# Performance work log

Hardware: AMD Instinct MI355X
Metric: run time of the kernel (lower is better)

Reference implementation:

```python
import jax, jax.numpy as jnp
import numpy as np

B, L, H, P = 4, 8192, 256, 256


def discretize(log_real, imag, log_Delta, B_real, B_imag):
    # Lambda = -exp(log_real) + i*imag ; ZOH discretization
    Lr = -jnp.exp(log_real)
    Li = imag
    Delta = jnp.exp(log_Delta)
    ad = Lr * Delta
    bd = Li * Delta
    exp_ad = jnp.exp(ad)
    Lbar_r = exp_ad * jnp.cos(bd)
    Lbar_i = exp_ad * jnp.sin(bd)
    denom = jnp.maximum(Lr * Lr + Li * Li, 1e-12)
    inv_Lr = Lr / denom
    inv_Li = -Li / denom
    diff_r = Lbar_r - 1.0
    diff_i = Lbar_i
    coeff_r = inv_Lr * diff_r - inv_Li * diff_i
    coeff_i = inv_Lr * diff_i + inv_Li * diff_r
    B_bar_r = coeff_r[:, None] * B_real - coeff_i[:, None] * B_imag
    B_bar_i = coeff_r[:, None] * B_imag + coeff_i[:, None] * B_real
    return Lbar_r, Lbar_i, B_bar_r, B_bar_i


def binop(ei, ej):
    Ar_i, Ai_i, xr_i, xi_i = ei
    Ar_j, Ai_j, xr_j, xi_j = ej
    return (Ar_j * Ar_i - Ai_j * Ai_i,
            Ar_j * Ai_i + Ai_j * Ar_i,
            Ar_j * xr_i - Ai_j * xi_i + xr_j,
            Ar_j * xi_i + Ai_j * xr_i + xi_j)


def apply_ssm(Lbar_r, Lbar_i, B_bar_r, B_bar_i, C_real, C_imag, D, x):
    # x: (B,L,H), B_bar: (P,H), C: (H,P)
    Bu_r = jnp.einsum('blh,ph->blp', x, B_bar_r)
    Bu_i = jnp.einsum('blh,ph->blp', x, B_bar_i)
    A_r = jnp.broadcast_to(Lbar_r, Bu_r.shape)
    A_i = jnp.broadcast_to(Lbar_i, Bu_i.shape)
    _, _, xs_r, xs_i = jax.lax.associative_scan(binop, (A_r, A_i, Bu_r, Bu_i), axis=1)
    ys = jnp.einsum('blp,hp->blh', xs_r, C_real) - jnp.einsum('blp,hp->blh', xs_i, C_imag)
    return ys + D * x


def s5(log_real, imag, log_Delta, B_real, B_imag, C_real, C_imag, D, x):
    Lbar_r, Lbar_i, B_bar_r, B_bar_i = discretize(log_real, imag, log_Delta, B_real, B_imag)
    y = apply_ssm(Lbar_r, Lbar_i, B_bar_r, B_bar_i, C_real, C_imag, D, x)
    return jax.nn.gelu(y, approximate=False)


def setup_inputs() -> dict:
    key = jax.random.key(0)
    ks = jax.random.split(key, 17)
    std_b = 1.0 / H ** 0.5
    std_c = 1.0 / P ** 0.5
    def params(ki):
        k = jax.random.split(ks[ki], 8)
        return dict(
            log_real=jax.random.normal(k[0], (P,), jnp.float32) * 0.5,
            imag=jax.random.normal(k[1], (P,), jnp.float32),
            log_Delta=jnp.zeros((P,), jnp.float32),
            B_real=jax.random.normal(k[2], (P, H), jnp.float32) * std_b,
            B_imag=jax.random.normal(k[3], (P, H), jnp.float32) * std_b,
            C_real=jax.random.normal(k[4], (H, P), jnp.float32) * std_c,
            C_imag=jax.random.normal(k[5], (H, P), jnp.float32) * std_c,
            D=jnp.ones((H,), jnp.float32),
        )
    f = params(1)
    b = params(2)
    inp = {'x': jax.random.normal(ks[0], (B, L, H), jnp.float32)}
    for name, v in f.items():
        inp['fwd_' + name] = v
    for name, v in b.items():
        inp['bwd_' + name] = v
    return inp


def reference(x,
              fwd_log_real, fwd_imag, fwd_log_Delta, fwd_B_real, fwd_B_imag,
              fwd_C_real, fwd_C_imag, fwd_D,
              bwd_log_real, bwd_imag, bwd_log_Delta, bwd_B_real, bwd_B_imag,
              bwd_C_real, bwd_C_imag, bwd_D):
    x_flip = jnp.flip(x, axis=1)
    y_f = s5(fwd_log_real, fwd_imag, fwd_log_Delta, fwd_B_real, fwd_B_imag,
             fwd_C_real, fwd_C_imag, fwd_D, x)
    y_b = s5(bwd_log_real, bwd_imag, bwd_log_Delta, bwd_B_real, bwd_B_imag,
             bwd_C_real, bwd_C_imag, bwd_D, x_flip)
    return y_f + jnp.flip(y_b, axis=1)
```

## Files before the change

kernel.cpp:

```cpp
#include <hip/hip_runtime.h>
#include <math.h>

#define B_DIM 4
#define L_DIM 8192
#define H_DIM 256
#define P_DIM 256
#define M_DIM (B_DIM * L_DIM)
#define NC 64
#define LC 128

typedef __attribute__((ext_vector_type(8))) short bf16x8;
typedef __attribute__((ext_vector_type(4))) float f32x4;

static __device__ __forceinline__ float bf2f(unsigned int u) {
    union { unsigned int i; float f; } v; v.i = u << 16; return v.f;
}
static __device__ __forceinline__ unsigned short f2bf(float f) {
    union { float f; unsigned int i; } v; v.f = f;
    unsigned int r = v.i + 0x7FFFu + ((v.i >> 16) & 1u);
    return (unsigned short)(r >> 16);
}
static __device__ __forceinline__ float gelu_f(float x) {
    float z = 0.7978845608028654f * (x + 0.044715f * x * x * x);
    float e = __expf(2.0f * z);
    float t = 1.0f - 2.0f / (e + 1.0f);
    return 0.5f * x * (1.0f + t);
}
static __device__ __forceinline__ void async_load16(const void* g, void* l) {
    __builtin_amdgcn_global_load_lds(
        (const __attribute__((address_space(1))) unsigned int*)g,
        (__attribute__((address_space(3))) unsigned int*)l, 16, 0, 0);
}
static __device__ __forceinline__ float2 cmul2(float2 a, float2 b) {
    return make_float2(a.x * b.x - a.y * b.y, a.x * b.y + a.y * b.x);
}
static __device__ __forceinline__ float2 csq2(float2 a) {
    return make_float2(a.x * a.x - a.y * a.y, 2.f * a.x * a.y);
}
static __device__ __forceinline__ float2 cmad(float2 A, float2 s, float2 z) {
    return make_float2(A.x * s.x - A.y * s.y + z.x, A.x * s.y + A.y * s.x + z.y);
}

__global__ void prep_kernel(const float* fLr, const float* fIm, const float* fLd,
                            const float* fBr, const float* fBi,
                            const float* fCr, const float* fCi,
                            const float* bLr, const float* bIm, const float* bLd,
                            const float* bBr, const float* bBi,
                            const float* bCr, const float* bCi,
                            const float4* __restrict__ x4, ushort4* __restrict__ xb,
                            unsigned short* Bmat, unsigned short* B3, float2* LbarWS) {
    int gid = blockIdx.x * 256 + threadIdx.x;
    if (gid < 2097152) {
        float4 v = x4[gid];
        ushort4 o;
        o.x = f2bf(v.x); o.y = f2bf(v.y); o.z = f2bf(v.z); o.w = f2bf(v.w);
        xb[gid] = o;
        return;
    }
    int g1 = gid - 2097152;
    if (g1 < 262144) {
        int k = g1 >> 8, h = g1 & 255;
        int d = k >> 9, pc = k & 511, p = pc >> 1, comp = pc & 1;
        const float* LR = d ? bLr : fLr;
        const float* IM = d ? bIm : fIm;
        const float* LD = d ? bLd : fLd;
        const float* BR = d ? bBr : fBr;
        const float* BI = d ? bBi : fBi;
        float Lr = -expf(LR[p]);
        float Li = IM[p];
        float Delta = expf(LD[p]);
        float ea = expf(Lr * Delta);
        float bd = Li * Delta;
        float Lbr = ea * cosf(bd);
        float Lbi = ea * sinf(bd);
        float denom = fmaxf(Lr * Lr + Li * Li, 1e-12f);
        float ivr = Lr / denom, ivi = -Li / denom;
        float dr = Lbr - 1.0f, di = Lbi;
        float cr = ivr * dr - ivi * di;
        float ci = ivr * di + ivi * dr;
        float br = BR[p * 256 + h], bi = BI[p * 256 + h];
        float val = comp ? (cr * bi + ci * br) : (cr * br - ci * bi);
        Bmat[g1] = f2bf(val);
    } else if (g1 < 524288) {
        int g2 = g1 - 262144;
        int d = g2 >> 17;
        int rem = g2 & 131071;
        int h = rem >> 9;
        int kk = rem & 511;
        int p = kk >> 1, comp = kk & 1;
        const float* CR = d ? bCr : fCr;
        const float* CI = d ? bCi : fCi;
        float val = comp ? -CI[h * 256 + p] : CR[h * 256 + p];
        B3[g2] = f2bf(val);
    } else if (g1 < 524800) {
        int g2 = g1 - 524288;
        int d = g2 >> 8, p = g2 & 255;
        const float* LR = d ? bLr : fLr;
        const float* IM = d ? bIm : fIm;
        const float* LD = d ? bLd : fLd;
        float Lr = -expf(LR[p]); float Li = IM[p]; float Delta = expf(LD[p]);
        float ea = expf(Lr * Delta); float bd = Li * Delta;
        LbarWS[g2] = make_float2(ea * cosf(bd), ea * sinf(bd));
    }
}

__global__ __launch_bounds__(256, 2) void k1_gemm(const unsigned short* __restrict__ A,
                                                  const unsigned short* __restrict__ Bm,
                                                  unsigned short* __restrict__ Bu,
                                                  const float2* __restrict__ Lbar,
                                                  float2* __restrict__ carry,
                                                  float2* __restrict__ Usub) {
    __shared__ unsigned short SH[16384];
    __shared__ float2 Sbuf2[64][4];
    int tid = threadIdx.x;
    int lane = tid & 63, wv = tid >> 6;
    int wm = (wv >> 1) * 64, wn = (wv & 1) * 64;
    int Mb = blockIdx.x * 128, Nb = blockIdx.y * 128;
    int lr = lane >> 3;
    int swz = ((lane & 7) ^ lr) * 8;
    f32x4 acc[4][4];
#pragma unroll
    for (int i = 0; i < 4; i++)
#pragma unroll
        for (int j = 0; j < 4; j++) acc[i][j] = (f32x4){0.f, 0.f, 0.f, 0.f};
    int mrow = lane & 15, quad = lane >> 4;
    for (int kb = 0; kb < 256; kb += 64) {
#pragma unroll
        for (int ch = wv; ch < 16; ch += 4) {
            int r = ch * 8 + lr;
            async_load16(A  + (size_t)(Mb + r) * 256 + kb + swz, (char*)SH + ch * 1024);
            async_load16(Bm + (size_t)(Nb + r) * 256 + kb + swz, (char*)SH + 16384 + ch * 1024);
        }
        __syncthreads();
#pragma unroll
        for (int kk = 0; kk < 64; kk += 32) {
            bf16x8 af[4], bfr[4];
#pragma unroll
            for (int i = 0; i < 4; i++) {
                int rr = wm + 16 * i + mrow;
                af[i] = *(const bf16x8*)&SH[rr * 64 + ((((kk >> 3) + quad) ^ (rr & 7)) << 3)];
            }
#pragma unroll
            for (int j = 0; j < 4; j++) {
                int rr = wn + 16 * j + mrow;
                bfr[j] = *(const bf16x8*)&SH[8192 + rr * 64 + ((((kk >> 3) + quad) ^ (rr & 7)) << 3)];
            }
#pragma unroll
            for (int i = 0; i < 4; i++)
#pragma unroll
                for (int j = 0; j < 4; j++)
                    acc[i][j] = __builtin_amdgcn_mfma_f32_16x16x32_bf16(af[i], bfr[j], acc[i][j], 0, 0, 0);
        }
        __syncthreads();
    }
    unsigned short* Cs = SH;
#pragma unroll
    for (int i = 0; i < 4; i++)
#pragma unroll
        for (int j = 0; j < 4; j++)
#pragma unroll
            for (int r = 0; r < 4; r++) {
                int row = wm + 16 * i + quad * 4 + r;
                int col = wn + 16 * j + mrow;
                Cs[row * 128 + col] = f2bf(acc[i][j][r]);
            }
    __syncthreads();
#pragma unroll
    for (int it = 0; it < 8; it++) {
        int o = tid * 16 + it * 4096;
        int row = o >> 8, colb = o & 255;
        uint4 v = *(const uint4*)((const char*)Cs + o);
        *(uint4*)((char*)Bu + (size_t)(Mb + row) * 2048 + (size_t)Nb * 2 + colb) = v;
    }
    int d = Nb >> 9;
    int b = Mb >> 13;
    int c = (Mb >> 7) & 63;
    float2 s = make_float2(0.f, 0.f);
    float2 A2 = make_float2(0.f, 0.f);
    float2 snap[3];
    snap[0] = snap[1] = snap[2] = make_float2(0.f, 0.f);
    int p = 0;
    if (tid < 128) {
        int j = tid & 63, half = tid >> 6;
        p = ((Nb & 511) >> 1) + j;
        A2 = Lbar[d * 256 + p];
        const unsigned int* C32 = (const unsigned int*)Cs;
        int r0 = half * 64;
        if (d == 0) {
            for (int t = 0; t < 64; t++) {
                unsigned int v = C32[(r0 + t) * 64 + j];
                float2 z = make_float2(bf2f(v & 0xffffu), bf2f(v >> 16));
                s = cmad(A2, s, z);
                if ((t & 15) == 15 && t < 63) snap[t >> 4] = s;
            }
        } else {
            for (int t = 63; t >= 0; t--) {
                unsigned int v = C32[(r0 + t) * 64 + j];
                float2 z = make_float2(bf2f(v & 0xffffu), bf2f(v >> 16));
                s = cmad(A2, s, z);
                if ((t & 15) == 0 && t > 0) snap[(t >> 4) - 1] = s;
            }
        }
        if (half == 1) {
            Sbuf2[j][0] = snap[0]; Sbuf2[j][1] = snap[1];
            Sbuf2[j][2] = snap[2]; Sbuf2[j][3] = s;
        }
    }
    __syncthreads();
    if (tid < 64) {
        float2 h1a = Sbuf2[tid][0], h1b = Sbuf2[tid][1], h1c = Sbuf2[tid][2], S1 = Sbuf2[tid][3];
        float2 a16 = A2;
#pragma unroll
        for (int k = 0; k < 4; k++) a16 = csq2(a16);
        float2 a32 = csq2(a16);
        float2 a48 = cmul2(a32, a16);
        float2 a64 = csq2(a32);
        float2 S0 = s;
        float2 Uq[8];
        float2 cfull;
        float2 zero = make_float2(0.f, 0.f);
        if (d == 0) {
            Uq[0] = zero;  Uq[1] = snap[0]; Uq[2] = snap[1]; Uq[3] = snap[2];
            Uq[4] = S0;
            Uq[5] = cmad(a16, S0, h1a);
            Uq[6] = cmad(a32, S0, h1b);
            Uq[7] = cmad(a48, S0, h1c);
            cfull = cmad(a64, S0, S1);
        } else {
            Uq[7] = zero;
            Uq[6] = h1c;
            Uq[5] = h1b;
            Uq[4] = h1a;
            Uq[3] = S1;
            Uq[2] = cmad(a16, S1, snap[2]);
            Uq[1] = cmad(a32, S1, snap[1]);
            Uq[0] = cmad(a48, S1, snap[0]);
            cfull = cmad(a64, S1, S0);
        }
        size_t cidx = ((size_t)(d * 4 + b) * NC + c) * 256 + p;
        carry[cidx] = cfull;
        size_t ub = (((size_t)(d * 4 + b) * NC + c) * 8) * 256 + p;
#pragma unroll
        for (int q = 0; q < 8; q++) Usub[ub + (size_t)q * 256] = Uq[q];
    }
}

static __device__ __forceinline__ void k3_half(const unsigned short* __restrict__ XS,
                                               const unsigned short* __restrict__ B3h,
                                               unsigned short* As, unsigned short* Bs,
                                               float2* UL, const float2* Ptab, const float2* LbarL,
                                               const float2* __restrict__ Uchunk,
                                               int Mb, int Hb, int coff, int d,
                                               int wm, int wn, int mrow, int quad,
                                               int lr, int swz, int wv, int tid,
                                               f32x4 (&acc)[4][4]) {
#pragma unroll
    for (int it = 0; it < 4; it++)
        async_load16((const char*)Uchunk + (size_t)(wv * 4 + it) * 1024 + (size_t)(tid & 63) * 16,
                     (char*)UL + (wv * 4 + it) * 1024);
    int j = tid & 31, q = tid >> 5;
    int r0 = q * 16;
    for (int kb = 0; kb < 512; kb += 64) {
#pragma unroll
        for (int ch = wv; ch < 16; ch += 4) {
            int r = ch * 8 + lr;
            async_load16(XS + (size_t)(Mb + r) * 1024 + coff + kb + swz, (char*)As + ch * 1024);
            async_load16(B3h + (size_t)(Hb + r) * 512 + kb + swz, (char*)Bs + ch * 1024);
        }
        __syncthreads();
        {
            int p = (kb >> 1) + j;
            float2 Ac = LbarL[d * 256 + p];
            float2 P  = Ptab[d * 256 + p];
            float2 U  = UL[q * 256 + p];
            int e = d ? (7 - q) : q;
            float2 ap = make_float2(1.f, 0.f);
            float2 bp = Ac;
#pragma unroll
            for (int k = 0; k < 4; k++) bp = csq2(bp);
            if (e & 1) ap = cmul2(ap, bp);
            bp = csq2(bp);
            if (e & 2) ap = cmul2(ap, bp);
            bp = csq2(bp);
            if (e & 4) ap = cmul2(ap, bp);
            float2 s = cmad(ap, P, U);
            unsigned int* A32 = (unsigned int*)As;
            unsigned int zb[16];
#pragma unroll
            for (int t = 0; t < 16; t++) {
                int row = r0 + t;
                zb[t] = A32[row * 32 + (((j >> 2) ^ (row & 7)) << 2) + (j & 3)];
            }
            if (d == 0) {
#pragma unroll
                for (int t = 0; t < 16; t++) {
                    float2 z = make_float2(bf2f(zb[t] & 0xffffu), bf2f(zb[t] >> 16));
                    s = cmad(Ac, s, z);
                    zb[t] = (unsigned int)f2bf(s.x) | ((unsigned int)f2bf(s.y) << 16);
                }
            } else {
#pragma unroll
                for (int t = 15; t >= 0; t--) {
                    float2 z = make_float2(bf2f(zb[t] & 0xffffu), bf2f(zb[t] >> 16));
                    s = cmad(Ac, s, z);
                    zb[t] = (unsigned int)f2bf(s.x) | ((unsigned int)f2bf(s.y) << 16);
                }
            }
#pragma unroll
            for (int t = 0; t < 16; t++) {
                int row = r0 + t;
                A32[row * 32 + (((j >> 2) ^ (row & 7)) << 2) + (j & 3)] = zb[t];
            }
        }
        __syncthreads();
#pragma unroll
        for (int kk = 0; kk < 64; kk += 32) {
            bf16x8 af[4], bfr[4];
#pragma unroll
            for (int i = 0; i < 4; i++) {
                int rr = wm + 16 * i + mrow;
                af[i] = *(const bf16x8*)&As[rr * 64 + ((((kk >> 3) + quad) ^ (rr & 7)) << 3)];
            }
#pragma unroll
            for (int jj2 = 0; jj2 < 4; jj2++) {
                int rr = wn + 16 * jj2 + mrow;
                bfr[jj2] = *(const bf16x8*)&Bs[rr * 64 + ((((kk >> 3) + quad) ^ (rr & 7)) << 3)];
            }
#pragma unroll
            for (int i = 0; i < 4; i++)
#pragma unroll
                for (int jj2 = 0; jj2 < 4; jj2++)
                    acc[i][jj2] = __builtin_amdgcn_mfma_f32_16x16x32_bf16(af[i], bfr[jj2], acc[i][jj2], 0, 0, 0);
        }
        __syncthreads();
    }
}

__global__ __launch_bounds__(256, 2) void k3_gemm(const unsigned short* __restrict__ XS,
                                                  const unsigned short* __restrict__ B3,
                                                  const unsigned short* __restrict__ xbf,
                                                  const float* __restrict__ Df,
                                                  const float* __restrict__ Db,
                                                  const float2* __restrict__ Lbar,
                                                  const float2* __restrict__ carry,
                                                  const float2* __restrict__ Usub,
                                                  float* __restrict__ out) {
    __shared__ unsigned short As[128 * 64];
    __shared__ unsigned short Bs[128 * 64];
    __shared__ float2 UL[2048];
    __shared__ float2 Ptab[512];
    __shared__ float2 LbarL[512];
    int tid = threadIdx.x;
    int lane = tid & 63, wv = tid >> 6;
    int wm = (wv >> 1) * 64, wn = (wv & 1) * 64;
    int Mb = blockIdx.x * 128, Hb = blockIdx.y * 128;
    int b = Mb >> 13, c = (Mb >> 7) & 63;
    int lr = lane >> 3;
    int swz = ((lane & 7) ^ lr) * 8;
    int mrow = lane & 15, quad = lane >> 4;
    {
        int p0 = tid;
#pragma unroll
        for (int d2 = 0; d2 < 2; d2++) {
            float2 A = Lbar[d2 * 256 + p0];
            LbarL[d2 * 256 + p0] = A;
            float2 a128 = A;
#pragma unroll
            for (int k = 0; k < 7; k++) a128 = csq2(a128);
            float2 s = make_float2(0.f, 0.f);
            const float2* cb = carry + ((size_t)(d2 * 4 + b) * NC) * 256 + p0;
            if (d2 == 0) {
#pragma unroll 16
                for (int jj = 0; jj < c; jj++) s = cmad(a128, s, cb[(size_t)jj * 256]);
            } else {
#pragma unroll 16
                for (int jj = NC - 1; jj > c; jj--) s = cmad(a128, s, cb[(size_t)jj * 256]);
            }
            Ptab[d2 * 256 + p0] = s;
        }
    }
    __syncthreads();
    f32x4 accf[4][4], accb[4][4];
#pragma unroll
    for (int i = 0; i < 4; i++)
#pragma unroll
        for (int j = 0; j < 4; j++) {
            accf[i][j] = (f32x4){0.f, 0.f, 0.f, 0.f};
            accb[i][j] = (f32x4){0.f, 0.f, 0.f, 0.f};
        }
    const float2* U0 = Usub + (((size_t)(0 * 4 + b) * NC + c) * 8) * 256;
    const float2* U1 = Usub + (((size_t)(1 * 4 + b) * NC + c) * 8) * 256;
    k3_half(XS, B3,          As, Bs, UL, Ptab, LbarL, U0, Mb, Hb, 0,   0,
            wm, wn, mrow, quad, lr, swz, wv, tid, accf);
    k3_half(XS, B3 + 131072, As, Bs, UL, Ptab, LbarL, U1, Mb, Hb, 512, 1,
            wm, wn, mrow, quad, lr, swz, wv, tid, accb);
#pragma unroll
    for (int i = 0; i < 4; i++)
#pragma unroll
        for (int j = 0; j < 4; j++) {
            int h = Hb + wn + 16 * j + mrow;
            float df = Df[h], db = Db[h];
#pragma unroll
            for (int r = 0; r < 4; r++) {
                int row = Mb + wm + 16 * i + quad * 4 + r;
                float xv = bf2f((unsigned int)xbf[(size_t)row * 256 + h]);
                float yf = accf[i][j][r] + df * xv;
                float yb = accb[i][j][r] + db * xv;
                out[(size_t)row * 256 + h] = gelu_f(yf) + gelu_f(yb);
            }
        }
}

extern "C" void kernel_launch(void* const* d_in, const int* in_sizes, int n_in,
                              void* d_out, int out_size, void* d_ws, size_t ws_size,
                              hipStream_t stream) {
    const float* x   = (const float*)d_in[0];
    const float* fLr = (const float*)d_in[1];
    const float* fIm = (const float*)d_in[2];
    const float* fLd = (const float*)d_in[3];
    const float* fBr = (const float*)d_in[4];
    const float* fBi = (const float*)d_in[5];
    const float* fCr = (const float*)d_in[6];
    const float* fCi = (const float*)d_in[7];
    const float* fD  = (const float*)d_in[8];
    const float* bLr = (const float*)d_in[9];
    const float* bIm = (const float*)d_in[10];
    const float* bLd = (const float*)d_in[11];
    const float* bBr = (const float*)d_in[12];
    const float* bBi = (const float*)d_in[13];
    const float* bCr = (const float*)d_in[14];
    const float* bCi = (const float*)d_in[15];
    const float* bD  = (const float*)d_in[16];
    float* out = (float*)d_out;

    char* ws = (char*)d_ws;
    unsigned short* xbf  = (unsigned short*)(ws);
    unsigned short* Bu   = (unsigned short*)(ws + 16777216);
    unsigned short* Bmat = (unsigned short*)(ws + 16777216 + 67108864);
    unsigned short* B3   = (unsigned short*)(ws + 16777216 + 67108864 + 524288);
    float2* LbarWS = (float2*)(ws + 16777216 + 67108864 + 1048576);
    float2* carry  = (float2*)(ws + 16777216 + 67108864 + 1048576 + 4096);
    float2* Usub   = (float2*)(ws + 16777216 + 67108864 + 1048576 + 4096 + 1048576);

    prep_kernel<<<10242, 256, 0, stream>>>(fLr, fIm, fLd, fBr, fBi, fCr, fCi,
                                           bLr, bIm, bLd, bBr, bBi, bCr, bCi,
                                           (const float4*)x, (ushort4*)xbf,
                                           Bmat, B3, LbarWS);
    k1_gemm<<<dim3(256, 8), 256, 0, stream>>>(xbf, Bmat, Bu, LbarWS, carry, Usub);
    k3_gemm<<<dim3(256, 2), 256, 0, stream>>>(Bu, B3, xbf, fD, bD, LbarWS, carry, Usub, out);
}
```

Measured before the change: 199.4 us.

## Double-buffer k3 GEMM shared tiles and prefetch U from global into registers

```diff
diff --git a/kernel.cpp b/kernel.cpp
--- a/kernel.cpp
+++ b/kernel.cpp
@@ -247,69 +247,79 @@
 
 static __device__ __forceinline__ void k3_half(const unsigned short* __restrict__ XS,
                                                const unsigned short* __restrict__ B3h,
-                                               unsigned short* As, unsigned short* Bs,
-                                               float2* UL, const float2* Ptab, const float2* LbarL,
+                                               unsigned short* As0, unsigned short* Bs0,
+                                               unsigned short* As1, unsigned short* Bs1,
+                                               const float2* Ptab, const float2* LbarL,
                                                const float2* __restrict__ Uchunk,
                                                int Mb, int Hb, int coff, int d,
                                                int wm, int wn, int mrow, int quad,
                                                int lr, int swz, int wv, int tid,
                                                f32x4 (&acc)[4][4]) {
-#pragma unroll
-    for (int it = 0; it < 4; it++)
-        async_load16((const char*)Uchunk + (size_t)(wv * 4 + it) * 1024 + (size_t)(tid & 63) * 16,
-                     (char*)UL + (wv * 4 + it) * 1024);
     int j = tid & 31, q = tid >> 5;
     int r0 = q * 16;
-    for (int kb = 0; kb < 512; kb += 64) {
-#pragma unroll
-        for (int ch = wv; ch < 16; ch += 4) {
-            int r = ch * 8 + lr;
-            async_load16(XS + (size_t)(Mb + r) * 1024 + coff + kb + swz, (char*)As + ch * 1024);
-            async_load16(B3h + (size_t)(Hb + r) * 512 + kb + swz, (char*)Bs + ch * 1024);
-        }
+    const float2* ubase = Uchunk + q * 256 + j;
+#define STAGE_K3(KB, AB, BB)                                                                  \
+    do {                                                                                      \
+        _Pragma("unroll")                                                                     \
+        for (int ch = wv; ch < 16; ch += 4) {                                                 \
+            int r = ch * 8 + lr;                                                              \
+            async_load16(XS + (size_t)(Mb + r) * 1024 + coff + (KB) + swz, (char*)(AB) + ch * 1024); \
+            async_load16(B3h + (size_t)(Hb + r) * 512 + (KB) + swz, (char*)(BB) + ch * 1024); \
+        }                                                                                     \
+    } while (0)
+    STAGE_K3(0, As0, Bs0);
+    float2 Ucur = ubase[0];
+    for (int st = 0; st < 8; st++) {
+        int kb = st * 64;
+        unsigned short* Ac = (st & 1) ? As1 : As0;
+        unsigned short* Bc = (st & 1) ? Bs1 : Bs0;
         __syncthreads();
+        float2 Unext = Ucur;
+        if (st < 7) {
+            STAGE_K3(kb + 64, (st & 1) ? As0 : As1, (st & 1) ? Bs0 : Bs1);
+            Unext = ubase[(kb + 64) >> 1];
+        }
         {
             int p = (kb >> 1) + j;
-            float2 Ac = LbarL[d * 256 + p];
+            float2 Ach = LbarL[d * 256 + p];
             float2 P  = Ptab[d * 256 + p];
-            float2 U  = UL[q * 256 + p];
             int e = d ? (7 - q) : q;
+            float2 bp = Ach;
+#pragma unroll
+            for (int k = 0; k < 4; k++) bp = csq2(bp);
             float2 ap = make_float2(1.f, 0.f);
-            float2 bp = Ac;
-#pragma unroll
-            for (int k = 0; k < 4; k++) bp = csq2(bp);
             if (e & 1) ap = cmul2(ap, bp);
             bp = csq2(bp);
             if (e & 2) ap = cmul2(ap, bp);
             bp = csq2(bp);
             if (e & 4) ap = cmul2(ap, bp);
-            float2 s = cmad(ap, P, U);
-            unsigned int* A32 = (unsigned int*)As;
+            float2 sv = cmad(ap, P, Ucur);
+            unsigned int* A32 = (unsigned int*)Ac;
             unsigned int zb[16];
 #pragma unroll
-            for (int t = 0; t < 16; t++) {
-                int row = r0 + t;
-                zb[t] = A32[row * 32 + (((j >> 2) ^ (row & 7)) << 2) + (j & 3)];
+            for (int tt = 0; tt < 16; tt++) {
+                int row = r0 + tt;
+                zb[tt] = A32[row * 32 + (((j >> 2) ^ (row & 7)) << 2) + (j & 3)];
             }
             if (d == 0) {
 #pragma unroll
-                for (int t = 0; t < 16; t++) {
-                    float2 z = make_float2(bf2f(zb[t] & 0xffffu), bf2f(zb[t] >> 16));
-                    s = cmad(Ac, s, z);
-                    zb[t] = (unsigned int)f2bf(s.x) | ((unsigned int)f2bf(s.y) << 16);
+                for (int tt = 0; tt < 16; tt++) {
+                    float2 z = make_float2(bf2f(zb[tt] & 0xffffu), bf2f(zb[tt] >> 16));
+                    sv = cmad(Ach, sv, z);
+                    zb[tt] = (unsigned int)f2bf(sv.x) | ((unsigned int)f2bf(sv.y) << 16);
                 }
             } else {
 #pragma unroll
-                for (int t = 15; t >= 0; t--) {
-                    float2 z = make_float2(bf2f(zb[t] & 0xffffu), bf2f(zb[t] >> 16));
-                    s = cmad(Ac, s, z);
-                    zb[t] = (unsigned int)f2bf(s.x) | ((unsigned int)f2bf(s.y) << 16);
+                for (int tt = 15; tt >= 0; tt--) {
+                    float2 z = make_float2(bf2f(zb[tt] & 0xffffu), bf2f(zb[tt] >> 16));
+                    sv = cmad(Ach, sv, z);
+                    zb[tt] = (unsigned int)f2bf(sv.x) | ((unsigned int)f2bf(sv.y) << 16);
                 }
             }
 #pragma unroll
-            for (int t = 0; t < 16; t++) {
-                int row = r0 + t;
-                A32[row * 32 + (((j >> 2) ^ (row & 7)) << 2) + (j & 3)] = zb[t];
+            for (int tt = 0; tt < 16; tt++) {
+                int row = r0 + tt;
+                A32[row * 32 + (((j >> 2) ^ (row & 7)) << 2) + (j & 3)] = zb[tt];
             }
         }
         __syncthreads();
@@ -319,12 +329,12 @@
 #pragma unroll
             for (int i = 0; i < 4; i++) {
                 int rr = wm + 16 * i + mrow;
-                af[i] = *(const bf16x8*)&As[rr * 64 + ((((kk >> 3) + quad) ^ (rr & 7)) << 3)];
+                af[i] = *(const bf16x8*)&Ac[rr * 64 + ((((kk >> 3) + quad) ^ (rr & 7)) << 3)];
             }
 #pragma unroll
             for (int jj2 = 0; jj2 < 4; jj2++) {
                 int rr = wn + 16 * jj2 + mrow;
-                bfr[jj2] = *(const bf16x8*)&Bs[rr * 64 + ((((kk >> 3) + quad) ^ (rr & 7)) << 3)];
+                bfr[jj2] = *(const bf16x8*)&Bc[rr * 64 + ((((kk >> 3) + quad) ^ (rr & 7)) << 3)];
             }
 #pragma unroll
             for (int i = 0; i < 4; i++)
@@ -332,8 +342,9 @@
                 for (int jj2 = 0; jj2 < 4; jj2++)
                     acc[i][jj2] = __builtin_amdgcn_mfma_f32_16x16x32_bf16(af[i], bfr[jj2], acc[i][jj2], 0, 0, 0);
         }
-        __syncthreads();
-    }
+        Ucur = Unext;
+    }
+#undef STAGE_K3
 }
 
 __global__ __launch_bounds__(256, 2) void k3_gemm(const unsigned short* __restrict__ XS,
@@ -345,9 +356,8 @@
                                                   const float2* __restrict__ carry,
                                                   const float2* __restrict__ Usub,
                                                   float* __restrict__ out) {
-    __shared__ unsigned short As[128 * 64];
-    __shared__ unsigned short Bs[128 * 64];
-    __shared__ float2 UL[2048];
+    __shared__ unsigned short As0[8192], Bs0[8192];
+    __shared__ unsigned short As1[8192], Bs1[8192];
     __shared__ float2 Ptab[512];
     __shared__ float2 LbarL[512];
     int tid = threadIdx.x;
@@ -390,9 +400,9 @@
         }
     const float2* U0 = Usub + (((size_t)(0 * 4 + b) * NC + c) * 8) * 256;
     const float2* U1 = Usub + (((size_t)(1 * 4 + b) * NC + c) * 8) * 256;
-    k3_half(XS, B3,          As, Bs, UL, Ptab, LbarL, U0, Mb, Hb, 0,   0,
+    k3_half(XS, B3,          As0, Bs0, As1, Bs1, Ptab, LbarL, U0, Mb, Hb, 0,   0,
             wm, wn, mrow, quad, lr, swz, wv, tid, accf);
-    k3_half(XS, B3 + 131072, As, Bs, UL, Ptab, LbarL, U1, Mb, Hb, 512, 1,
+    k3_half(XS, B3 + 131072, As0, Bs0, As1, Bs1, Ptab, LbarL, U1, Mb, Hb, 512, 1,
             wm, wn, mrow, quad, lr, swz, wv, tid, accb);
 #pragma unroll
     for (int i = 0; i < 4; i++)
```

Result: faster. 193.2 us (-3.1%).
